# Kernel tuning notes

Measured on AMD Instinct MI355X. Metric: run time of the kernel, lower is better.

## Reference

```python
import jax, jax.numpy as jnp
import numpy as np

CONTEXT_DIM = 512
HIDDEN = 1024
NUM_HEADS = 16
HEAD_DIM = HIDDEN // NUM_HEADS  # 64
ROTARY_DIM = int(HEAD_DIM * 0.25)  # 16
ROPE_BASE = 10000.0


def setup_inputs() -> dict:
    key = jax.random.key(0)
    ks = jax.random.split(key, 9)
    s = 0.02
    return {
        "context": jax.random.normal(ks[0], (2, 2048, CONTEXT_DIM), dtype=jnp.float32),
        "Wq": jax.random.normal(ks[1], (CONTEXT_DIM, HIDDEN), dtype=jnp.float32) * s,
        "bq": jnp.zeros((HIDDEN,), dtype=jnp.float32),
        "Wk": jax.random.normal(ks[2], (CONTEXT_DIM, HIDDEN), dtype=jnp.float32) * s,
        "bk": jnp.zeros((HIDDEN,), dtype=jnp.float32),
        "Wv": jax.random.normal(ks[3], (CONTEXT_DIM, HIDDEN), dtype=jnp.float32) * s,
        "bv": jnp.zeros((HIDDEN,), dtype=jnp.float32),
        "Wd": jax.random.normal(ks[4], (HIDDEN, HIDDEN), dtype=jnp.float32) * s,
        "bd": jnp.zeros((HIDDEN,), dtype=jnp.float32),
    }


def _rope_tables(seq_len, dtype):
    # GPT-NeoX style: inv_freq over even indices, emb = cat(freqs, freqs)
    inv_freq = 1.0 / (ROPE_BASE ** (jnp.arange(0, ROTARY_DIM, 2, dtype=jnp.float32) / ROTARY_DIM))
    t = jnp.arange(seq_len, dtype=jnp.float32)
    freqs = t[:, None] * inv_freq[None, :]           # [S, R/2]
    emb = jnp.concatenate([freqs, freqs], axis=-1)   # [S, R]
    return jnp.cos(emb).astype(dtype), jnp.sin(emb).astype(dtype)


def _rotate_half(x):
    x1, x2 = jnp.split(x, 2, axis=-1)
    return jnp.concatenate([-x2, x1], axis=-1)


def _attention(context, Wq, bq, Wk, bk, Wv, bv, Wd, bd):
    B, S, _ = context.shape
    q = (context @ Wq + bq).reshape(B, S, NUM_HEADS, HEAD_DIM).transpose(0, 2, 1, 3)
    k = (context @ Wk + bk).reshape(B, S, NUM_HEADS, HEAD_DIM).transpose(0, 2, 1, 3)
    v = (context @ Wv + bv).reshape(B, S, NUM_HEADS, HEAD_DIM).transpose(0, 2, 1, 3)

    cos, sin = _rope_tables(S, q.dtype)              # [S, R]
    cos = cos[None, None, :, :]
    sin = sin[None, None, :, :]

    def rope(x):
        xr, xp = x[..., :ROTARY_DIM], x[..., ROTARY_DIM:]
        xr = xr * cos + _rotate_half(xr) * sin
        return jnp.concatenate([xr, xp], axis=-1)

    q = rope(q)
    k = rope(k)

    scale = HEAD_DIM ** -0.5
    scores = jnp.einsum("bhqd,bhkd->bhqk", q, k) * scale  # [B,H,S,S]
    causal = jnp.arange(S)[:, None] >= jnp.arange(S)[None, :]
    scores = jnp.where(causal[None, None], scores, -jnp.inf)
    probs = jax.nn.softmax(scores, axis=-1)
    out = jnp.einsum("bhqk,bhkd->bhqd", probs, v)         # [B,H,S,D]
    out = out.transpose(0, 2, 1, 3).reshape(B, S, HIDDEN)
    return out @ Wd + bd


def reference(context, Wq, bq, Wk, bk, Wv, bv, Wd, bd):
    return _attention(context, Wq, bq, Wk, bk, Wv, bv, Wd, bd)
```

## Files before the change

### kernel.cpp

```cpp
#include <hip/hip_runtime.h>
#include <math.h>

#define NB   2
#define SEQ  2048
#define CDIM 512
#define HID  1024
#define NH   16
#define HD   64

typedef __attribute__((ext_vector_type(8))) short short8;
typedef __attribute__((ext_vector_type(4))) float f32x4;

__device__ __forceinline__ unsigned short f2b(float f) {
    union { float f; unsigned int u; } x; x.f = f;
    unsigned int r = x.u + 0x7fffu + ((x.u >> 16) & 1u);
    return (unsigned short)(r >> 16);
}
__device__ __forceinline__ float b2f(unsigned short s) {
    union { unsigned int u; float f; } x; x.u = ((unsigned int)s) << 16;
    return x.f;
}

__global__ __launch_bounds__(256)
void pack_ctx(const float* __restrict__ src, unsigned short* __restrict__ dst)
{
    const int idx = blockIdx.x * 256 + threadIdx.x;
    const float4 a = *(const float4*)&src[(size_t)idx * 4];
    ushort4 o;
    o.x = f2b(a.x); o.y = f2b(a.y); o.z = f2b(a.z); o.w = f2b(a.w);
    *(ushort4*)&dst[(size_t)idx * 4] = o;
}

__global__ __launch_bounds__(256)
void packT(const float* __restrict__ s0, const float* __restrict__ s1,
           const float* __restrict__ s2,
           unsigned short* __restrict__ d0, unsigned short* __restrict__ d1,
           unsigned short* __restrict__ d2, int K, int N)
{
    const int z = blockIdx.z;
    const float* __restrict__ src = (z == 0) ? s0 : ((z == 1) ? s1 : s2);
    unsigned short* __restrict__ dst = (z == 0) ? d0 : ((z == 1) ? d1 : d2);

    __shared__ unsigned short Lt[64][72];
    const int tid = threadIdx.x;
    const int k0 = blockIdx.x * 64;
    const int n0 = blockIdx.y * 64;
    #pragma unroll
    for (int it = 0; it < 4; it++) {
        const int ch  = tid + it * 256;
        const int row = ch >> 4;
        const int c4  = (ch & 15) * 4;
        const float4 a = *(const float4*)&src[(size_t)(k0 + row) * N + n0 + c4];
        Lt[c4 + 0][row] = f2b(a.x);
        Lt[c4 + 1][row] = f2b(a.y);
        Lt[c4 + 2][row] = f2b(a.z);
        Lt[c4 + 3][row] = f2b(a.w);
    }
    __syncthreads();
    #pragma unroll
    for (int it = 0; it < 4; it++) {
        const int ch = tid + it * 256;
        const int d  = ch >> 4;
        const int k4 = (ch & 15) * 4;
        ushort4 o;
        o.x = Lt[d][k4 + 0]; o.y = Lt[d][k4 + 1];
        o.z = Lt[d][k4 + 2]; o.w = Lt[d][k4 + 3];
        *(ushort4*)&dst[(size_t)(n0 + d) * K + k0 + k4] = o;
    }
}

__global__ __launch_bounds__(256)
void qkv_mfma(const unsigned short* __restrict__ Ab,
              const unsigned short* __restrict__ wqt,
              const unsigned short* __restrict__ wkt,
              const unsigned short* __restrict__ wvt,
              const float* __restrict__ bq, const float* __restrict__ bk,
              const float* __restrict__ bv,
              unsigned short* __restrict__ qo, unsigned short* __restrict__ ko,
              unsigned short* __restrict__ vo)
{
    const int z = blockIdx.z;
    const unsigned short* __restrict__ Bt = (z == 0) ? wqt : ((z == 1) ? wkt : wvt);
    const float* __restrict__ bias        = (z == 0) ? bq  : ((z == 1) ? bk  : bv);
    unsigned short* __restrict__ out      = (z == 0) ? qo  : ((z == 1) ? ko  : vo);
    const float scl = (z == 0) ? 0.125f : 1.0f;

    __shared__ unsigned short As[128 * 64];
    __shared__ unsigned short Bs[64 * 64];

    const int tid  = threadIdx.x;
    const int lane = tid & 63;
    const int wid  = tid >> 6;
    const int wr   = wid >> 1, wc = wid & 1;
    const int lr   = lane & 15, lk = lane >> 4;
    const int bm   = blockIdx.x * 128;
    const int h    = blockIdx.y;

    const f32x4 z4 = {0.f, 0.f, 0.f, 0.f};
    f32x4 acc[4][2];
    #pragma unroll
    for (int m = 0; m < 4; m++) { acc[m][0] = z4; acc[m][1] = z4; }

    for (int kt = 0; kt < CDIM / 64; kt++) {
        __syncthreads();
        #pragma unroll
        for (int it = 0; it < 4; it++) {
            const int ch = tid + it * 256;
            const int row = ch >> 3, slot = ch & 7;
            *(short8*)&As[row * 64 + ((slot ^ (row & 7)) << 3)] =
                *(const short8*)&Ab[(size_t)(bm + row) * CDIM + kt * 64 + slot * 8];
        }
        #pragma unroll
        for (int it = 0; it < 2; it++) {
            const int ch = tid + it * 256;
            const int row = ch >> 3, slot = ch & 7;
            *(short8*)&Bs[row * 64 + ((slot ^ (row & 7)) << 3)] =
                *(const short8*)&Bt[(size_t)(h * 64 + row) * CDIM + kt * 64 + slot * 8];
        }
        __syncthreads();
        const int sw = (lr & 7) << 3;
        #pragma unroll
        for (int ks = 0; ks < 2; ks++) {
            short8 bfr[2], afr[4];
            #pragma unroll
            for (int n = 0; n < 2; n++)
                bfr[n] = *(const short8*)&Bs[(wc * 32 + n * 16 + lr) * 64 + ((ks * 32 + lk * 8) ^ sw)];
            #pragma unroll
            for (int m = 0; m < 4; m++)
                afr[m] = *(const short8*)&As[(wr * 64 + m * 16 + lr) * 64 + ((ks * 32 + lk * 8) ^ sw)];
            #pragma unroll
            for (int m = 0; m < 4; m++)
                #pragma unroll
                for (int n = 0; n < 2; n++)
                    acc[m][n] = __builtin_amdgcn_mfma_f32_16x16x32_bf16(afr[m], bfr[n], acc[m][n], 0, 0, 0);
        }
    }

    #pragma unroll
    for (int m = 0; m < 4; m++) {
        #pragma unroll
        for (int g = 0; g < 4; g++) {
            const int mrow = bm + wr * 64 + m * 16 + lk * 4 + g;
            const int b_ = mrow >> 11;
            const int s  = mrow & (SEQ - 1);
            #pragma unroll
            for (int n = 0; n < 2; n++) {
                const int d = wc * 32 + n * 16 + lr;
                out[(((size_t)(b_ * NH + h)) * SEQ + s) * HD + d] =
                    f2b((acc[m][n][g] + bias[h * 64 + d]) * scl);
            }
        }
    }
}

__global__ __launch_bounds__(256)
void rope_bf16(unsigned short* __restrict__ q, unsigned short* __restrict__ k)
{
    const int idx = blockIdx.x * 256 + threadIdx.x;
    const int per = NB * NH * SEQ * 8;
    unsigned short* x;
    int r;
    if (idx < per) { x = q; r = idx; } else { x = k; r = idx - per; }
    const int i  = r & 7;
    const int s  = (r >> 3) & (SEQ - 1);
    const int bh = r >> 14;
    unsigned short* p = x + ((size_t)bh * SEQ + s) * HD;
    const float inv_freq = exp2f((float)i * (-13.287712379549449f / 8.0f));
    float sn, cs;
    sincosf((float)s * inv_freq, &sn, &cs);
    const float x1 = b2f(p[i]), x2 = b2f(p[i + 8]);
    p[i]     = f2b(fmaf(x1, cs, -x2 * sn));
    p[i + 8] = f2b(fmaf(x2, cs,  x1 * sn));
}

__global__ __launch_bounds__(256)
void pack_v(const unsigned short* __restrict__ v, unsigned short* __restrict__ vt)
{
    __shared__ unsigned short Lt[64][72];
    const int tid  = threadIdx.x;
    const int tile = blockIdx.x;
    const int bh   = blockIdx.y;
    const size_t ibase = ((size_t)bh * SEQ + tile * 64) * HD;
    #pragma unroll
    for (int it = 0; it < 4; it++) {
        const int ch  = tid + it * 256;
        const int row = ch >> 4;
        const int c4  = (ch & 15) * 4;
        const ushort4 a = *(const ushort4*)&v[ibase + (size_t)row * HD + c4];
        Lt[c4 + 0][row] = a.x;
        Lt[c4 + 1][row] = a.y;
        Lt[c4 + 2][row] = a.z;
        Lt[c4 + 3][row] = a.w;
    }
    __syncthreads();
    const size_t obase = (size_t)bh * HD * SEQ + tile * 64;
    #pragma unroll
    for (int it = 0; it < 4; it++) {
        const int ch = tid + it * 256;
        const int d  = ch >> 4;
        const int s4 = (ch & 15) * 4;
        ushort4 o;
        o.x = Lt[d][s4 + 0]; o.y = Lt[d][s4 + 1];
        o.z = Lt[d][s4 + 2]; o.w = Lt[d][s4 + 3];
        *(ushort4*)&vt[obase + (size_t)d * SEQ + s4] = o;
    }
}

__global__ __launch_bounds__(256)
void attn_mfma(const unsigned short* __restrict__ qg,
               const unsigned short* __restrict__ kg,
               const unsigned short* __restrict__ vtg,
               unsigned short* __restrict__ out)
{
    __shared__ unsigned short Ks[64 * 64];
    __shared__ unsigned short Vs[64 * 64];
    __shared__ unsigned short Ps[4][16 * 64];

    const int tid  = threadIdx.x;
    const int lane = tid & 63;
    const int wv   = tid >> 6;
    const int p    = blockIdx.x;
    const int h    = blockIdx.y, b = blockIdx.z;
    const size_t base = ((size_t)(b * NH + h)) * SEQ * HD;

    const int lr = lane & 15;
    const int lk = lane >> 4;

    const int ch0 = tid * 2, ch1 = tid * 2 + 1;
    const int r0 = ch0 >> 3, sl0 = ch0 & 7;
    const int r1 = ch1 >> 3, sl1 = ch1 & 7;
    const int dd0 = r0 * 64 + ((sl0 ^ (r0 & 7)) << 3);
    const int dd1 = r1 * 64 + ((sl1 ^ (r1 & 7)) << 3);

    const f32x4 z4 = {0.f, 0.f, 0.f, 0.f};

    #pragma unroll
    for (int half = 0; half < 2; half++) {
        const int T  = half ? (31 - p) : p;
        const int q0 = T * 64;

        const int qrow = q0 + wv * 16 + lr;
        const short8 qf0 = *(const short8*)&qg[base + (size_t)qrow * HD + lk * 8];
        const short8 qf1 = *(const short8*)&qg[base + (size_t)qrow * HD + 32 + lk * 8];

        f32x4 o[4] = {z4, z4, z4, z4};
        float mrun = -3.0e38f, lrun = 0.f;

        short8 kp0 = *(const short8*)&kg[base + (size_t)r0 * HD + sl0 * 8];
        short8 kp1 = *(const short8*)&kg[base + (size_t)r1 * HD + sl1 * 8];
        short8 vp0 = *(const short8*)&vtg[base + (size_t)r0 * SEQ + sl0 * 8];
        short8 vp1 = *(const short8*)&vtg[base + (size_t)r1 * SEQ + sl1 * 8];

        for (int kb = 0; kb <= T; kb++) {
            __syncthreads();
            *(short8*)&Ks[dd0] = kp0;
            *(short8*)&Ks[dd1] = kp1;
            *(short8*)&Vs[dd0] = vp0;
            *(short8*)&Vs[dd1] = vp1;
            if (kb < T) {
                const int kn = kb + 1;
                kp0 = *(const short8*)&kg[base + (size_t)(kn * 64 + r0) * HD + sl0 * 8];
                kp1 = *(const short8*)&kg[base + (size_t)(kn * 64 + r1) * HD + sl1 * 8];
                vp0 = *(const short8*)&vtg[base + (size_t)r0 * SEQ + kn * 64 + sl0 * 8];
                vp1 = *(const short8*)&vtg[base + (size_t)r1 * SEQ + kn * 64 + sl1 * 8];
            }
            __syncthreads();

            f32x4 s[4] = {z4, z4, z4, z4};
            #pragma unroll
            for (int nt = 0; nt < 4; nt++) {
                const int krow = nt * 16 + lr;
                const int sw   = (krow & 7) << 3;
                const short8 kf0 = *(const short8*)&Ks[krow * 64 + ((lk * 8) ^ sw)];
                const short8 kf1 = *(const short8*)&Ks[krow * 64 + ((32 + lk * 8) ^ sw)];
                s[nt] = __builtin_amdgcn_mfma_f32_16x16x32_bf16(kf0, qf0, s[nt], 0, 0, 0);
                s[nt] = __builtin_amdgcn_mfma_f32_16x16x32_bf16(kf1, qf1, s[nt], 0, 0, 0);
            }

            if (kb == T) {
                #pragma unroll
                for (int nt = 0; nt < 4; nt++)
                    #pragma unroll
                    for (int g = 0; g < 4; g++)
                        if (nt * 16 + lk * 4 + g > wv * 16 + lr) s[nt][g] = -3.0e38f;
            }

            float mx = -3.0e38f;
            #pragma unroll
            for (int nt = 0; nt < 4; nt++)
                #pragma unroll
                for (int g = 0; g < 4; g++) mx = fmaxf(mx, s[nt][g]);
            mx = fmaxf(mx, __shfl_xor(mx, 16));
            mx = fmaxf(mx, __shfl_xor(mx, 32));
            const float mn   = fmaxf(mrun, mx);
            const float corr = __expf(mrun - mn);
            mrun = mn;
            float pp[4][4];
            float rs = 0.f;
            #pragma unroll
            for (int nt = 0; nt < 4; nt++)
                #pragma unroll
                for (int g = 0; g < 4; g++) { pp[nt][g] = __expf(s[nt][g] - mn); rs += pp[nt][g]; }
            rs += __shfl_xor(rs, 16);
            rs += __shfl_xor(rs, 32);
            lrun = lrun * corr + rs;

            #pragma unroll
            for (int g = 0; g < 4; g++) {
                const float cg = __shfl(corr, lk * 4 + g);
                #pragma unroll
                for (int dt = 0; dt < 4; dt++) o[dt][g] *= cg;
            }

            const int psw = (lr & 7) << 3;
            #pragma unroll
            for (int nt = 0; nt < 4; nt++) {
                const int c0 = (nt * 16 + lk * 4) ^ psw;
                const unsigned int w01 = (unsigned int)f2b(pp[nt][0]) | ((unsigned int)f2b(pp[nt][1]) << 16);
                const unsigned int w23 = (unsigned int)f2b(pp[nt][2]) | ((unsigned int)f2b(pp[nt][3]) << 16);
                *(unsigned int*)&Ps[wv][lr * 64 + c0]     = w01;
                *(unsigned int*)&Ps[wv][lr * 64 + c0 + 2] = w23;
            }
            asm volatile("s_waitcnt lgkmcnt(0)" ::: "memory");

            #pragma unroll
            for (int ks = 0; ks < 2; ks++) {
                const short8 pf = *(const short8*)&Ps[wv][lr * 64 + ((ks * 32 + lk * 8) ^ psw)];
                #pragma unroll
                for (int dt = 0; dt < 4; dt++) {
                    const int vrow = dt * 16 + lr;
                    const short8 vf = *(const short8*)&Vs[vrow * 64 + ((ks * 32 + lk * 8) ^ psw)];
                    o[dt] = __builtin_amdgcn_mfma_f32_16x16x32_bf16(pf, vf, o[dt], 0, 0, 0);
                }
            }
        }

        #pragma unroll
        for (int g = 0; g < 4; g++) {
            const int qr = q0 + wv * 16 + lk * 4 + g;
            const float lg  = __shfl(lrun, lk * 4 + g);
            const float inv = 1.0f / lg;
            unsigned short* op = &out[((size_t)(b * SEQ + qr)) * HID + h * HD + lr];
            op[0]  = f2b(o[0][g] * inv);
            op[16] = f2b(o[1][g] * inv);
            op[32] = f2b(o[2][g] * inv);
            op[48] = f2b(o[3][g] * inv);
        }
    }
}

__global__ __launch_bounds__(256)
void proj_mfma(const unsigned short* __restrict__ Ab,
               const unsigned short* __restrict__ Bt,
               const float* __restrict__ bias, float* __restrict__ out)
{
    __shared__ unsigned short As[128 * 64];
    __shared__ unsigned short Bs[64 * 64];

    const int tid  = threadIdx.x;
    const int lane = tid & 63;
    const int wid  = tid >> 6;
    const int wr   = wid >> 1, wc = wid & 1;
    const int lr   = lane & 15, lk = lane >> 4;
    const int bm   = blockIdx.x * 128;
    const int bn   = blockIdx.y * 64;

    const f32x4 z4 = {0.f, 0.f, 0.f, 0.f};
    f32x4 acc[4][2];
    #pragma unroll
    for (int m = 0; m < 4; m++) { acc[m][0] = z4; acc[m][1] = z4; }

    for (int kt = 0; kt < HID / 64; kt++) {
        __syncthreads();
        #pragma unroll
        for (int it = 0; it < 4; it++) {
            const int ch = tid + it * 256;
            const int row = ch >> 3, slot = ch & 7;
            *(short8*)&As[row * 64 + ((slot ^ (row & 7)) << 3)] =
                *(const short8*)&Ab[(size_t)(bm + row) * HID + kt * 64 + slot * 8];
        }
        #pragma unroll
        for (int it = 0; it < 2; it++) {
            const int ch = tid + it * 256;
            const int row = ch >> 3, slot = ch & 7;
            *(short8*)&Bs[row * 64 + ((slot ^ (row & 7)) << 3)] =
                *(const short8*)&Bt[(size_t)(bn + row) * HID + kt * 64 + slot * 8];
        }
        __syncthreads();
        const int sw = (lr & 7) << 3;
        #pragma unroll
        for (int ks = 0; ks < 2; ks++) {
            short8 bfr[2], afr[4];
            #pragma unroll
            for (int n = 0; n < 2; n++)
                bfr[n] = *(const short8*)&Bs[(wc * 32 + n * 16 + lr) * 64 + ((ks * 32 + lk * 8) ^ sw)];
            #pragma unroll
            for (int m = 0; m < 4; m++)
                afr[m] = *(const short8*)&As[(wr * 64 + m * 16 + lr) * 64 + ((ks * 32 + lk * 8) ^ sw)];
            #pragma unroll
            for (int m = 0; m < 4; m++)
                #pragma unroll
                for (int n = 0; n < 2; n++)
                    acc[m][n] = __builtin_amdgcn_mfma_f32_16x16x32_bf16(afr[m], bfr[n], acc[m][n], 0, 0, 0);
        }
    }

    #pragma unroll
    for (int m = 0; m < 4; m++) {
        #pragma unroll
        for (int g = 0; g < 4; g++) {
            const int mrow = bm + wr * 64 + m * 16 + lk * 4 + g;
            #pragma unroll
            for (int n = 0; n < 2; n++) {
                const int ncol = bn + wc * 32 + n * 16 + lr;
                out[(size_t)mrow * HID + ncol] = acc[m][n][g] + bias[ncol];
            }
        }
    }
}

extern "C" void kernel_launch(void* const* d_in, const int* in_sizes, int n_in,
                              void* d_out, int out_size, void* d_ws, size_t ws_size,
                              hipStream_t stream)
{
    const float* ctx = (const float*)d_in[0];
    const float* Wq  = (const float*)d_in[1];
    const float* bq  = (const float*)d_in[2];
    const float* Wk  = (const float*)d_in[3];
    const float* bk  = (const float*)d_in[4];
    const float* Wv  = (const float*)d_in[5];
    const float* bv  = (const float*)d_in[6];
    const float* Wd  = (const float*)d_in[7];
    const float* bd  = (const float*)d_in[8];
    float* outp = (float*)d_out;

    char* w = (char*)d_ws;
    unsigned short* ctxb = (unsigned short*)(w);
    unsigned short* wqt  = (unsigned short*)(w + (size_t)4  * 1024 * 1024);
    unsigned short* wkt  = (unsigned short*)(w + (size_t)5  * 1024 * 1024);
    unsigned short* wvt  = (unsigned short*)(w + (size_t)6  * 1024 * 1024);
    unsigned short* wdt  = (unsigned short*)(w + (size_t)7  * 1024 * 1024);
    unsigned short* qb   = (unsigned short*)(w + (size_t)9  * 1024 * 1024);
    unsigned short* kb   = (unsigned short*)(w + (size_t)17 * 1024 * 1024);
    unsigned short* vb   = (unsigned short*)(w + (size_t)25 * 1024 * 1024);
    unsigned short* vt   = (unsigned short*)(w + (size_t)33 * 1024 * 1024);
    unsigned short* aw   = (unsigned short*)(w + (size_t)41 * 1024 * 1024);

    const dim3 blk(256);
    pack_ctx <<<dim3(2048),        blk, 0, stream>>>(ctx, ctxb);
    packT    <<<dim3(8, 16, 3),    blk, 0, stream>>>(Wq, Wk, Wv, wqt, wkt, wvt, CDIM, HID);
    packT    <<<dim3(16, 16, 1),   blk, 0, stream>>>(Wd, Wd, Wd, wdt, wdt, wdt, HID, HID);
    qkv_mfma <<<dim3(32, 16, 3),   blk, 0, stream>>>(ctxb, wqt, wkt, wvt, bq, bk, bv, qb, kb, vb);
    rope_bf16<<<dim3(4096),        blk, 0, stream>>>(qb, kb);
    pack_v   <<<dim3(32, 32),      blk, 0, stream>>>(vb, vt);
    attn_mfma<<<dim3(16, NH, NB),  blk, 0, stream>>>(qb, kb, vt, aw);
    proj_mfma<<<dim3(32, 16),      blk, 0, stream>>>(aw, wdt, bd, outp);
}
```

Baseline: 182.8 us.

## Merge pack kernels, write V transposed from QKV GEMM, use exp2 with lazy rescale

Merges the context cast and the three weight transpose-pack launches into one pack4 launch. The QKV GEMM now writes V directly in transposed layout, which removes the separate pack_v kernel and its intermediate buffer. In attention, log2(e) is folded into the Q scale so softmax can use raw v_exp_f32. The running max and output rescale are only updated when the new max exceeds the old one by more than a threshold, and probabilities are packed with hardware bf16 conversion. The lazy rescale lets exponentials reach up to 2^11 before renormalising, which carries some precision and overflow risk, and the transposed V writes are strided 8-byte stores.

```diff
diff --git a/kernel.cpp b/kernel.cpp
--- a/kernel.cpp
+++ b/kernel.cpp
@@ -16,41 +16,60 @@
     unsigned int r = x.u + 0x7fffu + ((x.u >> 16) & 1u);
     return (unsigned short)(r >> 16);
 }
+__device__ __forceinline__ unsigned int pk2(float a, float b) {
+    __bf16 x = (__bf16)a, y = (__bf16)b;
+    unsigned short ux = __builtin_bit_cast(unsigned short, x);
+    unsigned short uy = __builtin_bit_cast(unsigned short, y);
+    return (unsigned int)ux | ((unsigned int)uy << 16);
+}
 __device__ __forceinline__ float b2f(unsigned short s) {
     union { unsigned int u; float f; } x; x.u = ((unsigned int)s) << 16;
     return x.f;
 }
+__device__ __forceinline__ float fexp2(float x) {
+    float r;
+    asm("v_exp_f32 %0, %1" : "=v"(r) : "v"(x));
+    return r;
+}
 
 __global__ __launch_bounds__(256)
-void pack_ctx(const float* __restrict__ src, unsigned short* __restrict__ dst)
-{
-    const int idx = blockIdx.x * 256 + threadIdx.x;
-    const float4 a = *(const float4*)&src[(size_t)idx * 4];
-    ushort4 o;
-    o.x = f2b(a.x); o.y = f2b(a.y); o.z = f2b(a.z); o.w = f2b(a.w);
-    *(ushort4*)&dst[(size_t)idx * 4] = o;
-}
-
-__global__ __launch_bounds__(256)
-void packT(const float* __restrict__ s0, const float* __restrict__ s1,
-           const float* __restrict__ s2,
-           unsigned short* __restrict__ d0, unsigned short* __restrict__ d1,
-           unsigned short* __restrict__ d2, int K, int N)
-{
-    const int z = blockIdx.z;
-    const float* __restrict__ src = (z == 0) ? s0 : ((z == 1) ? s1 : s2);
-    unsigned short* __restrict__ dst = (z == 0) ? d0 : ((z == 1) ? d1 : d2);
+void pack4(const float* __restrict__ Wq, const float* __restrict__ Wk,
+           const float* __restrict__ Wv, const float* __restrict__ Wd,
+           const float* __restrict__ ctx,
+           unsigned short* __restrict__ wqt, unsigned short* __restrict__ wkt,
+           unsigned short* __restrict__ wvt, unsigned short* __restrict__ wdt,
+           unsigned short* __restrict__ ctxb)
+{
+    const int z   = blockIdx.z;
+    const int tid = threadIdx.x;
+
+    if (z == 4) {
+        const int blk = blockIdx.y * 16 + blockIdx.x;
+        #pragma unroll
+        for (int it = 0; it < 8; it++) {
+            const int idx = blk * 2048 + it * 256 + tid;
+            const float4 a = *(const float4*)&ctx[(size_t)idx * 4];
+            ushort4 o;
+            o.x = f2b(a.x); o.y = f2b(a.y); o.z = f2b(a.z); o.w = f2b(a.w);
+            *(ushort4*)&ctxb[(size_t)idx * 4] = o;
+        }
+        return;
+    }
+
+    const int K = (z == 3) ? HID : CDIM;
+    const int k0 = blockIdx.x * 64;
+    if (k0 >= K) return;
+    const int n0 = blockIdx.y * 64;
+    const float* __restrict__ src = (z == 0) ? Wq : ((z == 1) ? Wk : ((z == 2) ? Wv : Wd));
+    unsigned short* __restrict__ dst = (z == 0) ? wqt : ((z == 1) ? wkt : ((z == 2) ? wvt : wdt));
 
     __shared__ unsigned short Lt[64][72];
-    const int tid = threadIdx.x;
-    const int k0 = blockIdx.x * 64;
-    const int n0 = blockIdx.y * 64;
     #pragma unroll
     for (int it = 0; it < 4; it++) {
         const int ch  = tid + it * 256;
         const int row = ch >> 4;
         const int c4  = (ch & 15) * 4;
-        const float4 a = *(const float4*)&src[(size_t)(k0 + row) * N + n0 + c4];
+        const float4 a = *(const float4*)&src[(size_t)(k0 + row) * HID + n0 + c4];
         Lt[c4 + 0][row] = f2b(a.x);
         Lt[c4 + 1][row] = f2b(a.y);
         Lt[c4 + 2][row] = f2b(a.z);
@@ -77,13 +96,12 @@
               const float* __restrict__ bq, const float* __restrict__ bk,
               const float* __restrict__ bv,
               unsigned short* __restrict__ qo, unsigned short* __restrict__ ko,
-              unsigned short* __restrict__ vo)
+              unsigned short* __restrict__ vt)
 {
     const int z = blockIdx.z;
     const unsigned short* __restrict__ Bt = (z == 0) ? wqt : ((z == 1) ? wkt : wvt);
     const float* __restrict__ bias        = (z == 0) ? bq  : ((z == 1) ? bk  : bv);
-    unsigned short* __restrict__ out      = (z == 0) ? qo  : ((z == 1) ? ko  : vo);
-    const float scl = (z == 0) ? 0.125f : 1.0f;
+    const float scl = (z == 0) ? 0.125f * 1.44269504f : 1.0f;
 
     __shared__ unsigned short As[128 * 64];
     __shared__ unsigned short Bs[64 * 64];
@@ -136,18 +154,39 @@
         }
     }
 
-    #pragma unroll
-    for (int m = 0; m < 4; m++) {
-        #pragma unroll
-        for (int g = 0; g < 4; g++) {
-            const int mrow = bm + wr * 64 + m * 16 + lk * 4 + g;
-            const int b_ = mrow >> 11;
-            const int s  = mrow & (SEQ - 1);
+    if (z < 2) {
+        unsigned short* __restrict__ out = (z == 0) ? qo : ko;
+        #pragma unroll
+        for (int m = 0; m < 4; m++) {
+            #pragma unroll
+            for (int g = 0; g < 4; g++) {
+                const int mrow = bm + wr * 64 + m * 16 + lk * 4 + g;
+                const int b_ = mrow >> 11;
+                const int s  = mrow & (SEQ - 1);
+                #pragma unroll
+                for (int n = 0; n < 2; n++) {
+                    const int d = wc * 32 + n * 16 + lr;
+                    out[(((size_t)(b_ * NH + h)) * SEQ + s) * HD + d] =
+                        f2b((acc[m][n][g] + bias[h * 64 + d]) * scl);
+                }
+            }
+        }
+    } else {
+        #pragma unroll
+        for (int m = 0; m < 4; m++) {
+            const int mrow0 = bm + wr * 64 + m * 16 + lk * 4;
+            const int b_ = mrow0 >> 11;
+            const int s0 = mrow0 & (SEQ - 1);
             #pragma unroll
             for (int n = 0; n < 2; n++) {
                 const int d = wc * 32 + n * 16 + lr;
-                out[(((size_t)(b_ * NH + h)) * SEQ + s) * HD + d] =
-                    f2b((acc[m][n][g] + bias[h * 64 + d]) * scl);
+                const float bs = bias[h * 64 + d];
+                ushort4 o4;
+                o4.x = f2b(acc[m][n][0] + bs);
+                o4.y = f2b(acc[m][n][1] + bs);
+                o4.z = f2b(acc[m][n][2] + bs);
+                o4.w = f2b(acc[m][n][3] + bs);
+                *(ushort4*)&vt[(((size_t)(b_ * NH + h)) * HD + d) * SEQ + s0] = o4;
             }
         }
     }
@@ -174,39 +213,6 @@
 }
 
 __global__ __launch_bounds__(256)
-void pack_v(const unsigned short* __restrict__ v, unsigned short* __restrict__ vt)
-{
-    __shared__ unsigned short Lt[64][72];
-    const int tid  = threadIdx.x;
-    const int tile = blockIdx.x;
-    const int bh   = blockIdx.y;
-    const size_t ibase = ((size_t)bh * SEQ + tile * 64) * HD;
-    #pragma unroll
-    for (int it = 0; it < 4; it++) {
-        const int ch  = tid + it * 256;
-        const int row = ch >> 4;
-        const int c4  = (ch & 15) * 4;
-        const ushort4 a = *(const ushort4*)&v[ibase + (size_t)row * HD + c4];
-        Lt[c4 + 0][row] = a.x;
-        Lt[c4 + 1][row] = a.y;
-        Lt[c4 + 2][row] = a.z;
-        Lt[c4 + 3][row] = a.w;
-    }
-    __syncthreads();
-    const size_t obase = (size_t)bh * HD * SEQ + tile * 64;
-    #pragma unroll
-    for (int it = 0; it < 4; it++) {
-        const int ch = tid + it * 256;
-        const int d  = ch >> 4;
-        const int s4 = (ch & 15) * 4;
-        ushort4 o;
-        o.x = Lt[d][s4 + 0]; o.y = Lt[d][s4 + 1];
-        o.z = Lt[d][s4 + 2]; o.w = Lt[d][s4 + 3];
-        *(ushort4*)&vt[obase + (size_t)d * SEQ + s4] = o;
-    }
-}
-
-__global__ __launch_bounds__(256)
 void attn_mfma(const unsigned short* __restrict__ qg,
                const unsigned short* __restrict__ kg,
                const unsigned short* __restrict__ vtg,
@@ -292,34 +298,36 @@
                 for (int g = 0; g < 4; g++) mx = fmaxf(mx, s[nt][g]);
             mx = fmaxf(mx, __shfl_xor(mx, 16));
             mx = fmaxf(mx, __shfl_xor(mx, 32));
-            const float mn   = fmaxf(mrun, mx);
-            const float corr = __expf(mrun - mn);
-            mrun = mn;
+
+            float corr = 1.0f;
+            if (__any(mx > mrun + 11.0f)) {
+                const float mn = fmaxf(mrun, mx);
+                corr = fexp2(mrun - mn);
+                mrun = mn;
+                #pragma unroll
+                for (int g = 0; g < 4; g++) {
+                    const float cg = __shfl(corr, lk * 4 + g);
+                    #pragma unroll
+                    for (int dt = 0; dt < 4; dt++) o[dt][g] *= cg;
+                }
+            }
+
             float pp[4][4];
             float rs = 0.f;
             #pragma unroll
             for (int nt = 0; nt < 4; nt++)
                 #pragma unroll
-                for (int g = 0; g < 4; g++) { pp[nt][g] = __expf(s[nt][g] - mn); rs += pp[nt][g]; }
+                for (int g = 0; g < 4; g++) { pp[nt][g] = fexp2(s[nt][g] - mrun); rs += pp[nt][g]; }
             rs += __shfl_xor(rs, 16);
             rs += __shfl_xor(rs, 32);
             lrun = lrun * corr + rs;
 
-            #pragma unroll
-            for (int g = 0; g < 4; g++) {
-                const float cg = __shfl(corr, lk * 4 + g);
-                #pragma unroll
-                for (int dt = 0; dt < 4; dt++) o[dt][g] *= cg;
-            }
-
             const int psw = (lr & 7) << 3;
             #pragma unroll
             for (int nt = 0; nt < 4; nt++) {
                 const int c0 = (nt * 16 + lk * 4) ^ psw;
-                const unsigned int w01 = (unsigned int)f2b(pp[nt][0]) | ((unsigned int)f2b(pp[nt][1]) << 16);
-                const unsigned int w23 = (unsigned int)f2b(pp[nt][2]) | ((unsigned int)f2b(pp[nt][3]) << 16);
-                *(unsigned int*)&Ps[wv][lr * 64 + c0]     = w01;
-                *(unsigned int*)&Ps[wv][lr * 64 + c0 + 2] = w23;
+                *(unsigned int*)&Ps[wv][lr * 64 + c0]     = pk2(pp[nt][0], pp[nt][1]);
+                *(unsigned int*)&Ps[wv][lr * 64 + c0 + 2] = pk2(pp[nt][2], pp[nt][3]);
             }
             asm volatile("s_waitcnt lgkmcnt(0)" ::: "memory");
 
@@ -442,17 +450,13 @@
     unsigned short* wdt  = (unsigned short*)(w + (size_t)7  * 1024 * 1024);
     unsigned short* qb   = (unsigned short*)(w + (size_t)9  * 1024 * 1024);
     unsigned short* kb   = (unsigned short*)(w + (size_t)17 * 1024 * 1024);
-    unsigned short* vb   = (unsigned short*)(w + (size_t)25 * 1024 * 1024);
-    unsigned short* vt   = (unsigned short*)(w + (size_t)33 * 1024 * 1024);
-    unsigned short* aw   = (unsigned short*)(w + (size_t)41 * 1024 * 1024);
+    unsigned short* vt   = (unsigned short*)(w + (size_t)25 * 1024 * 1024);
+    unsigned short* aw   = (unsigned short*)(w + (size_t)33 * 1024 * 1024);
 
     const dim3 blk(256);
-    pack_ctx <<<dim3(2048),        blk, 0, stream>>>(ctx, ctxb);
-    packT    <<<dim3(8, 16, 3),    blk, 0, stream>>>(Wq, Wk, Wv, wqt, wkt, wvt, CDIM, HID);
-    packT    <<<dim3(16, 16, 1),   blk, 0, stream>>>(Wd, Wd, Wd, wdt, wdt, wdt, HID, HID);
-    qkv_mfma <<<dim3(32, 16, 3),   blk, 0, stream>>>(ctxb, wqt, wkt, wvt, bq, bk, bv, qb, kb, vb);
-    rope_bf16<<<dim3(4096),        blk, 0, stream>>>(qb, kb);
-    pack_v   <<<dim3(32, 32),      blk, 0, stream>>>(vb, vt);
-    attn_mfma<<<dim3(16, NH, NB),  blk, 0, stream>>>(qb, kb, vt, aw);
-    proj_mfma<<<dim3(32, 16),      blk, 0, stream>>>(aw, wdt, bd, outp);
-}
+    pack4    <<<dim3(16, 16, 5),  blk, 0, stream>>>(Wq, Wk, Wv, Wd, ctx, wqt, wkt, wvt, wdt, ctxb);
+    qkv_mfma <<<dim3(32, 16, 3),  blk, 0, stream>>>(ctxb, wqt, wkt, wvt, bq, bk, bv, qb, kb, vt);
+    rope_bf16<<<dim3(4096),       blk, 0, stream>>>(qb, kb);
+    attn_mfma<<<dim3(16, NH, NB), blk, 0, stream>>>(qb, kb, vt, aw);
+    proj_mfma<<<dim3(32, 16),     blk, 0, stream>>>(aw, wdt, bd, outp);
+}
```

Result: faster. 171.5 us (-6.2%).
